# Kernel tuning notes

Measured on AMD Instinct MI355X. Metric: run time of the kernel, lower is better.

## Reference

```python
import jax, jax.numpy as jnp
import numpy as np

T, B, IN, H, L = 512, 32, 512, 512, 2  # seq_len, batch, input_size, hidden_size, num_layers
D = 2  # bidirectional
EPS = 1e-5


def setup_inputs() -> dict:
    key = jax.random.key(0)
    ks = jax.random.split(key, 4)
    s = 0.05
    return {
        "x": jax.random.normal(ks[0], (T, B, IN), jnp.float32),
        "h0": jnp.zeros((L * D, B, H), jnp.float32),
        # stacked per (layer, direction) params; index = 2*layer + dir (dir 0 = fwd, 1 = back)
        "Wx": jax.random.normal(ks[1], (L * D, IN, 3 * H), jnp.float32) * s,
        "Wh": jax.random.normal(ks[2], (L * D, H, 3 * H), jnp.float32) * s,
        "bx": jnp.zeros((L * D, 3 * H), jnp.float32),
        "bh": jnp.zeros((L * D, 3 * H), jnp.float32),
        "gx": jnp.ones((L * D, 3 * H), jnp.float32),   # LN affine scale for input proj
        "bex": jnp.zeros((L * D, 3 * H), jnp.float32), # LN affine shift for input proj
        "gh": jnp.ones((L * D, 3 * H), jnp.float32),   # LN affine scale for recurrent proj
        "beh": jnp.zeros((L * D, 3 * H), jnp.float32), # LN affine shift for recurrent proj
    }


def _ln3(a, g, b):
    # per-gate LayerNorm: a is [B, 3H]; normalize each H-sized gate chunk
    Bn, H3 = a.shape
    Hh = H3 // 3
    a = a.reshape(Bn, 3, Hh)
    mu = a.mean(-1, keepdims=True)
    var = ((a - mu) ** 2).mean(-1, keepdims=True)
    a = (a - mu) * jax.lax.rsqrt(var + EPS)
    a = a * g.reshape(3, Hh) + b.reshape(3, Hh)
    return a.reshape(Bn, H3)


def _run_dir(xs, h, Wx, Wh, bx, bh, gx, bex, gh, beh):
    # xs: [T, B, F], h: [B, H]; scan LNGRU cell over time
    def step(h, x):
        ax = _ln3(x @ Wx + bx, gx, bex)
        ah = _ln3(h @ Wh + bh, gh, beh)
        axr, axz, axn = jnp.split(ax, 3, axis=-1)
        ahr, ahz, ahn = jnp.split(ah, 3, axis=-1)
        r = jax.nn.sigmoid(axr + ahr)
        z = jax.nn.sigmoid(axz + ahz)
        n = jnp.tanh(axn + r * ahn)
        h_new = (1.0 - z) * n + z * h
        return h_new, h_new
    hT, ys = jax.lax.scan(step, h, xs)
    return hT, ys


def reference(x, h0, Wx, Wh, bx, bh, gx, bex, gh, beh):
    ff, back = x, x
    hiddens = []
    for layer in range(L):
        i = 2 * layer
        hT, ff = _run_dir(ff, h0[i], Wx[i], Wh[i], bx[i], bh[i], gx[i], bex[i], gh[i], beh[i])
        hiddens.append(hT)
        j = 2 * layer + 1
        hT, yb = _run_dir(back[::-1], h0[j], Wx[j], Wh[j], bx[j], bh[j], gx[j], bex[j], gh[j], beh[j])
        back = yb[::-1]
        hiddens.append(hT)
    output = jnp.concatenate([ff, back], axis=-1)  # [T, B, 2H]
    return output, jnp.stack(hiddens)  # hiddens: [L*2, B, H]
```

## Files before the change

kernel.cpp:

```cpp
#include <hip/hip_runtime.h>

#define T_N 512
#define B_N 32
#define H_N 512
#define G3 1536
#define NBLK 192
#define NGRP 8
#define GRPSZ (NBLK / NGRP)
#define NT 1024
#define EPS_LN 1e-5f
#define OUT_HID_OFF (T_N * B_N * 1024)

#define WS_STATS 320
#define WS_DOTS  (WS_STATS + 1536)
#define WS_HBUF  (WS_DOTS + 4 * B_N * G3)
#define WS_Y0    (WS_HBUF + 2 * B_N * H_N)

#define WLDS_F 32256
#define HL_F   8256
#define LDS_BYTES ((WLDS_F + HL_F + 256) * 4)

__device__ __forceinline__ float cload(const float* p) {
  return __hip_atomic_load(p, __ATOMIC_RELAXED, __HIP_MEMORY_SCOPE_AGENT);
}
__device__ __forceinline__ void cstore(float* p, float v) {
  __hip_atomic_store(p, v, __ATOMIC_RELAXED, __HIP_MEMORY_SCOPE_AGENT);
}
union U64F2 { unsigned long long u; float f[2]; };
__device__ __forceinline__ U64F2 cload2(const float* p) {
  U64F2 r;
  r.u = __hip_atomic_load((const unsigned long long*)p, __ATOMIC_RELAXED,
                          __HIP_MEMORY_SCOPE_AGENT);
  return r;
}

__device__ __forceinline__ void gbar(unsigned* barbase, unsigned& epoch, int grp) {
  epoch++;
  __builtin_amdgcn_s_waitcnt(0);
  __syncthreads();
  if (threadIdx.x == 0) {
    unsigned* gc  = barbase + grp * 32;
    unsigned* top = barbase + NGRP * 32;
    unsigned* rel = barbase + NGRP * 32 + 32;
    unsigned r = __hip_atomic_fetch_add(gc, 1u, __ATOMIC_RELAXED, __HIP_MEMORY_SCOPE_AGENT);
    if (r == epoch * GRPSZ - 1u) {
      unsigned r2 = __hip_atomic_fetch_add(top, 1u, __ATOMIC_RELAXED, __HIP_MEMORY_SCOPE_AGENT);
      if (r2 == epoch * NGRP - 1u)
        __hip_atomic_store(rel, epoch, __ATOMIC_RELAXED, __HIP_MEMORY_SCOPE_AGENT);
    }
    while (__hip_atomic_load(rel, __ATOMIC_RELAXED, __HIP_MEMORY_SCOPE_AGENT) < epoch)
      __builtin_amdgcn_s_sleep(1);
  }
  __syncthreads();
}

__global__ void __launch_bounds__(NT, 1)
lngru5(const float* __restrict__ x, const float* __restrict__ h0,
       const float* __restrict__ Wx, const float* __restrict__ Wh,
       const float* __restrict__ bx, const float* __restrict__ bh,
       const float* __restrict__ gx, const float* __restrict__ bex,
       const float* __restrict__ gh, const float* __restrict__ beh,
       float* __restrict__ out, float* __restrict__ ws)
{
  extern __shared__ __align__(16) float smem[];
  float* wlds = smem;
  float* hl   = smem + WLDS_F;
  float* sred = smem + WLDS_F + HL_F;

  unsigned* barbase = (unsigned*)ws;
  float* stats = ws + WS_STATS;
  float* dots  = ws + WS_DOTS;
  float* hbuf  = ws + WS_HBUF;
  float* y0    = ws + WS_Y0;

  const int tid  = threadIdx.x;
  const int lane = tid & 63;
  const int wv   = tid >> 6;
  const int bid  = blockIdx.x;
  const int grp  = bid & 7;
  const int bs   = bid & 1;
  const int jt   = (bid >> 1) % 24;
  const int kd   = (bid >> 1) / 24;
  const int kind = kd & 1;
  const int d    = kd >> 1;
  const int j0   = jt * 64;
  const int g    = jt >> 3;
  const int b0   = bs * 16;
  const bool is_gate = (kind == 0) && (jt < 8);

  const int jq    = wv >> 1;
  const int bhf   = wv & 1;
  const int jj    = lane & 7;
  const int boct  = lane >> 3;
  const int b_loc = bhf * 8 + boct;
  const int b     = b0 + b_loc;
  const int jfull = j0 + jq * 8 + jj;

  unsigned epoch = 0;

  for (int ph = 0; ph < 2; ++ph) {
    const int widx = ph * 2 + d;

    const float* wgl = (kind ? Wh : Wx) + (size_t)widx * H_N * G3 + j0;
    for (int kk = 0; kk < 32; ++kk) {
      int k = wv * 32 + kk;
      if (k < 504)
        wlds[(k >> 2) * 256 + lane * 4 + (k & 3)] = wgl[(size_t)k * G3 + lane];
    }
    float wtail[8];
#pragma unroll
    for (int kk = 0; kk < 8; ++kk)
      wtail[kk] = wgl[(size_t)(504 + kk) * G3 + (jq * 8 + jj)];

    if (is_gate) {
      cstore(&hbuf[(d * B_N + b0 + wv) * H_N + j0 + lane],
             h0[(widx * B_N + b0 + wv) * H_N + j0 + lane]);
    }
    gbar(barbase, epoch, grp);

    const float  bv   = (kind ? bh : bx)[widx * G3 + jfull];
    const float* xsrc = (ph == 0) ? x : (y0 + (size_t)d * T_N * B_N * H_N);
    const float* hsrc = hbuf + (d * B_N + b0) * H_N;
    const float4* wq  = (const float4*)wlds + jq * 8 + jj;

    for (int s = 0; s < T_N; ++s) {
      const int t = d ? (T_N - 1 - s) : s;
      const int p = s & 1;
      float* stp = stats + p * 768;

      if (kind) {
#pragma unroll
        for (int q = 0; q < 4; ++q) {
          int e = (tid + q * 1024) * 2;
          U64F2 v = cload2(hsrc + e);
          int bb = e >> 9, k = e & 511;
          hl[bb * 516 + k]     = v.f[0];
          hl[bb * 516 + k + 1] = v.f[1];
        }
        __syncthreads();
      }

      float p0 = 0.f, p1 = 0.f, p2 = 0.f, p3 = 0.f;
      if (kind) {
        const float* hb = hl + b_loc * 516;
#pragma unroll 9
        for (int k4 = 0; k4 < 126; ++k4) {
          float4 w = wq[k4 * 64];
          float4 r = *(const float4*)(hb + k4 * 4);
          p0 = fmaf(r.x, w.x, p0);
          p1 = fmaf(r.y, w.y, p1);
          p2 = fmaf(r.z, w.z, p2);
          p3 = fmaf(r.w, w.w, p3);
        }
        float4 r1 = *(const float4*)(hb + 504);
        float4 r2 = *(const float4*)(hb + 508);
        p0 = fmaf(r1.x, wtail[0], p0); p1 = fmaf(r1.y, wtail[1], p1);
        p2 = fmaf(r1.z, wtail[2], p2); p3 = fmaf(r1.w, wtail[3], p3);
        p0 = fmaf(r2.x, wtail[4], p0); p1 = fmaf(r2.y, wtail[5], p1);
        p2 = fmaf(r2.z, wtail[6], p2); p3 = fmaf(r2.w, wtail[7], p3);
      } else {
        const float* rp = xsrc + ((size_t)t * B_N + b) * H_N;
#pragma unroll 9
        for (int k4 = 0; k4 < 126; ++k4) {
          float4 w = wq[k4 * 64];
          float4 r = *(const float4*)(rp + k4 * 4);
          p0 = fmaf(r.x, w.x, p0);
          p1 = fmaf(r.y, w.y, p1);
          p2 = fmaf(r.z, w.z, p2);
          p3 = fmaf(r.w, w.w, p3);
        }
        float4 r1 = *(const float4*)(rp + 504);
        float4 r2 = *(const float4*)(rp + 508);
        p0 = fmaf(r1.x, wtail[0], p0); p1 = fmaf(r1.y, wtail[1], p1);
        p2 = fmaf(r1.z, wtail[2], p2); p3 = fmaf(r1.w, wtail[3], p3);
        p0 = fmaf(r2.x, wtail[4], p0); p1 = fmaf(r2.y, wtail[5], p1);
        p2 = fmaf(r2.z, wtail[6], p2); p3 = fmaf(r2.w, wtail[7], p3);
      }
      float tot = bv + (p0 + p1) + (p2 + p3);

      cstore(&dots[(kd * B_N + b) * G3 + jfull], tot);

      float s1 = tot, s2 = tot * tot;
      s1 += __shfl_xor(s1, 1, 64); s2 += __shfl_xor(s2, 1, 64);
      s1 += __shfl_xor(s1, 2, 64); s2 += __shfl_xor(s2, 2, 64);
      s1 += __shfl_xor(s1, 4, 64); s2 += __shfl_xor(s2, 4, 64);
      if (jj == 0) {
        sred[(wv * 8 + boct) * 2 + 0] = s1;
        sred[(wv * 8 + boct) * 2 + 1] = s2;
      }
      __syncthreads();
      if (tid < 32) {
        int bl = tid >> 1, st = tid & 1;
        int bh2 = bl >> 3, bo2 = bl & 7;
        float a2 = 0.f;
#pragma unroll
        for (int q = 0; q < 8; ++q) a2 += sred[((q * 2 + bh2) * 8 + bo2) * 2 + st];
        atomicAdd(&stp[((kd * 3 + g) * B_N + b0 + bl) * 2 + st], a2);
      }

      gbar(barbase, epoch, grp);

      if (bid == NBLK - 1) {
        float* so = stats + (p ^ 1) * 768;
        if (tid < 768) cstore(so + tid, 0.f);
      }
      if (is_gate) {
        const int c  = j0 + lane;
        const int gb = b0 + wv;
        float a[2][3];
#pragma unroll
        for (int k2 = 0; k2 < 2; ++k2) {
          const float* dr  = dots + ((d * 2 + k2) * B_N + gb) * G3;
          const float* gam = (k2 ? gh : gx) + widx * G3;
          const float* bet = (k2 ? beh : bex) + widx * G3;
#pragma unroll
          for (int g2 = 0; g2 < 3; ++g2) {
            float v = cload(dr + g2 * H_N + c);
            const float* sl = stp + (((d * 2 + k2) * 3 + g2) * B_N + gb) * 2;
            float mu  = cload(sl)     * (1.f / 512.f);
            float var = cload(sl + 1) * (1.f / 512.f) - mu * mu;
            float inv = rsqrtf(var + EPS_LN);
            int J = g2 * H_N + c;
            a[k2][g2] = (v - mu) * inv * gam[J] + bet[J];
          }
        }
        float r = 1.f / (1.f + __expf(-(a[0][0] + a[1][0])));
        float z = 1.f / (1.f + __expf(-(a[0][1] + a[1][1])));
        float n = tanhf(a[0][2] + r * a[1][2]);
        float* hp = hbuf + (d * B_N + gb) * H_N + c;
        float hnew = (1.f - z) * n + z * cload(hp);
        cstore(hp, hnew);
        if (ph == 0) {
          cstore(&y0[(((size_t)d * T_N + t) * B_N + gb) * H_N + c], hnew);
        } else {
          out[((size_t)t * B_N + gb) * 1024 + d * H_N + c] = hnew;
        }
        if (s == T_N - 1) {
          out[OUT_HID_OFF + (widx * B_N + gb) * H_N + c] = hnew;
        }
      }
      gbar(barbase, epoch, grp);
    }
  }
}

extern "C" void kernel_launch(void* const* d_in, const int* in_sizes, int n_in,
                              void* d_out, int out_size, void* d_ws, size_t ws_size,
                              hipStream_t stream) {
  const float* x    = (const float*)d_in[0];
  const float* h0   = (const float*)d_in[1];
  const float* Wx   = (const float*)d_in[2];
  const float* Wh   = (const float*)d_in[3];
  const float* bxp  = (const float*)d_in[4];
  const float* bhp  = (const float*)d_in[5];
  const float* gxp  = (const float*)d_in[6];
  const float* bexp = (const float*)d_in[7];
  const float* ghp  = (const float*)d_in[8];
  const float* behp = (const float*)d_in[9];
  float* out = (float*)d_out;
  float* ws  = (float*)d_ws;

  hipMemsetAsync(d_ws, 0, 8192, stream);

  hipFuncSetAttribute((const void*)lngru5,
                      hipFuncAttributeMaxDynamicSharedMemorySize, LDS_BYTES);

  void* args[] = {(void*)&x, (void*)&h0, (void*)&Wx, (void*)&Wh, (void*)&bxp, (void*)&bhp,
                  (void*)&gxp, (void*)&bexp, (void*)&ghp, (void*)&behp, (void*)&out, (void*)&ws};
  hipLaunchCooperativeKernel((void*)lngru5, dim3(NBLK), dim3(NT), args, LDS_BYTES, stream);
}
```

Baseline: 26.25 ms.

## Split K across waves with 4x4 register tiles and LDS atomic reduction

Restructures the per-step matvec so each wave handles a slice of the K dimension and computes a 4x4 (j, batch) register tile, reusing each loaded weight and activation float4 across four outputs. Partial sums are combined through LDS atomics into a per-block accumulator. The x rows are now staged into LDS like the hidden state instead of being read straight from global memory per thread. This cuts LDS and global load traffic per FMA, at the cost of LDS atomic contention, an extra barrier, and uneven K splits across waves.

```diff
diff --git a/kernel.cpp b/kernel.cpp
--- a/kernel.cpp
+++ b/kernel.cpp
@@ -16,9 +16,11 @@
 #define WS_HBUF  (WS_DOTS + 4 * B_N * G3)
 #define WS_Y0    (WS_HBUF + 2 * B_N * H_N)
 
-#define WLDS_F 32256
+#define WLDS_F 31232
 #define HL_F   8256
-#define LDS_BYTES ((WLDS_F + HL_F + 256) * 4)
+#define PACC_F 1024
+#define SRED_F 128
+#define LDS_BYTES ((WLDS_F + HL_F + PACC_F + SRED_F) * 4)
 
 __device__ __forceinline__ float cload(const float* p) {
   return __hip_atomic_load(p, __ATOMIC_RELAXED, __HIP_MEMORY_SCOPE_AGENT);
@@ -54,8 +56,12 @@
   __syncthreads();
 }
 
+#define DOT4(A, W, R) A = fmaf((W).x, (R).x, fmaf((W).y, (R).y, fmaf((W).z, (R).z, fmaf((W).w, (R).w, A))))
+#define ACC4(I, W) do { DOT4(acc[I][0], W, r0); DOT4(acc[I][1], W, r1); \
+                        DOT4(acc[I][2], W, r2); DOT4(acc[I][3], W, r3); } while (0)
+
 __global__ void __launch_bounds__(NT, 1)
-lngru5(const float* __restrict__ x, const float* __restrict__ h0,
+lngru7(const float* __restrict__ x, const float* __restrict__ h0,
        const float* __restrict__ Wx, const float* __restrict__ Wh,
        const float* __restrict__ bx, const float* __restrict__ bh,
        const float* __restrict__ gx, const float* __restrict__ bex,
@@ -65,7 +71,8 @@
   extern __shared__ __align__(16) float smem[];
   float* wlds = smem;
   float* hl   = smem + WLDS_F;
-  float* sred = smem + WLDS_F + HL_F;
+  float* pacc = smem + WLDS_F + HL_F;
+  float* sred = smem + WLDS_F + HL_F + PACC_F;
 
   unsigned* barbase = (unsigned*)ws;
   float* stats = ws + WS_STATS;
@@ -88,29 +95,38 @@
   const int b0   = bs * 16;
   const bool is_gate = (kind == 0) && (jt < 8);
 
-  const int jq    = wv >> 1;
-  const int bhf   = wv & 1;
-  const int jj    = lane & 7;
-  const int boct  = lane >> 3;
-  const int b_loc = bhf * 8 + boct;
-  const int b     = b0 + b_loc;
-  const int jfull = j0 + jq * 8 + jj;
+  const int jg = lane & 15;
+  const int bg = lane >> 4;
+  const int cnt = (wv < 10) ? 8 : 7;
+  const int k40 = (wv < 10) ? (wv * 8) : (80 + (wv - 10) * 7);
+  const int tk0 = 488 + (wv - 10) * 4;
+
+  const int jlo = (tid & 15) * 4 + (tid >> 8);
+  const int blo = ((tid >> 4) & 3) * 4 + ((tid >> 6) & 3);
 
   unsigned epoch = 0;
 
   for (int ph = 0; ph < 2; ++ph) {
     const int widx = ph * 2 + d;
 
+    pacc[tid] = 0.f;
+
     const float* wgl = (kind ? Wh : Wx) + (size_t)widx * H_N * G3 + j0;
-    for (int kk = 0; kk < 32; ++kk) {
-      int k = wv * 32 + kk;
-      if (k < 504)
-        wlds[(k >> 2) * 256 + lane * 4 + (k & 3)] = wgl[(size_t)k * G3 + lane];
-    }
-    float wtail[8];
-#pragma unroll
-    for (int kk = 0; kk < 8; ++kk)
-      wtail[kk] = wgl[(size_t)(504 + kk) * G3 + (jq * 8 + jj)];
+    for (int e = tid; e < 488 * 64; e += NT) {
+      int k = e >> 6, jl = e & 63;
+      wlds[(k >> 2) * 256 + (jl & 3) * 64 + (jl >> 2) * 4 + (k & 3)] =
+          wgl[(size_t)k * G3 + jl];
+    }
+    float4 wt[4];
+    if (wv >= 10) {
+#pragma unroll
+      for (int i = 0; i < 4; ++i) {
+        wt[i].x = wgl[(size_t)(tk0 + 0) * G3 + jg * 4 + i];
+        wt[i].y = wgl[(size_t)(tk0 + 1) * G3 + jg * 4 + i];
+        wt[i].z = wgl[(size_t)(tk0 + 2) * G3 + jg * 4 + i];
+        wt[i].w = wgl[(size_t)(tk0 + 3) * G3 + jg * 4 + i];
+      }
+    }
 
     if (is_gate) {
       cstore(&hbuf[(d * B_N + b0 + wv) * H_N + j0 + lane],
@@ -118,10 +134,11 @@
     }
     gbar(barbase, epoch, grp);
 
-    const float  bv   = (kind ? bh : bx)[widx * G3 + jfull];
+    const float  bv   = (kind ? bh : bx)[widx * G3 + j0 + jlo];
     const float* xsrc = (ph == 0) ? x : (y0 + (size_t)d * T_N * B_N * H_N);
     const float* hsrc = hbuf + (d * B_N + b0) * H_N;
-    const float4* wq  = (const float4*)wlds + jq * 8 + jj;
+    const float4* wp4 = (const float4*)wlds;
+    const float*  hb0 = hl + (bg * 4) * 516;
 
     for (int s = 0; s < T_N; ++s) {
       const int t = d ? (T_N - 1 - s) : s;
@@ -134,67 +151,72 @@
           int e = (tid + q * 1024) * 2;
           U64F2 v = cload2(hsrc + e);
           int bb = e >> 9, k = e & 511;
-          hl[bb * 516 + k]     = v.f[0];
-          hl[bb * 516 + k + 1] = v.f[1];
-        }
-        __syncthreads();
-      }
-
-      float p0 = 0.f, p1 = 0.f, p2 = 0.f, p3 = 0.f;
-      if (kind) {
-        const float* hb = hl + b_loc * 516;
-#pragma unroll 9
-        for (int k4 = 0; k4 < 126; ++k4) {
-          float4 w = wq[k4 * 64];
-          float4 r = *(const float4*)(hb + k4 * 4);
-          p0 = fmaf(r.x, w.x, p0);
-          p1 = fmaf(r.y, w.y, p1);
-          p2 = fmaf(r.z, w.z, p2);
-          p3 = fmaf(r.w, w.w, p3);
-        }
-        float4 r1 = *(const float4*)(hb + 504);
-        float4 r2 = *(const float4*)(hb + 508);
-        p0 = fmaf(r1.x, wtail[0], p0); p1 = fmaf(r1.y, wtail[1], p1);
-        p2 = fmaf(r1.z, wtail[2], p2); p3 = fmaf(r1.w, wtail[3], p3);
-        p0 = fmaf(r2.x, wtail[4], p0); p1 = fmaf(r2.y, wtail[5], p1);
-        p2 = fmaf(r2.z, wtail[6], p2); p3 = fmaf(r2.w, wtail[7], p3);
+          *(float2*)(hl + bb * 516 + k) = make_float2(v.f[0], v.f[1]);
+        }
       } else {
-        const float* rp = xsrc + ((size_t)t * B_N + b) * H_N;
-#pragma unroll 9
-        for (int k4 = 0; k4 < 126; ++k4) {
-          float4 w = wq[k4 * 64];
-          float4 r = *(const float4*)(rp + k4 * 4);
-          p0 = fmaf(r.x, w.x, p0);
-          p1 = fmaf(r.y, w.y, p1);
-          p2 = fmaf(r.z, w.z, p2);
-          p3 = fmaf(r.w, w.w, p3);
-        }
-        float4 r1 = *(const float4*)(rp + 504);
-        float4 r2 = *(const float4*)(rp + 508);
-        p0 = fmaf(r1.x, wtail[0], p0); p1 = fmaf(r1.y, wtail[1], p1);
-        p2 = fmaf(r1.z, wtail[2], p2); p3 = fmaf(r1.w, wtail[3], p3);
-        p0 = fmaf(r2.x, wtail[4], p0); p1 = fmaf(r2.y, wtail[5], p1);
-        p2 = fmaf(r2.z, wtail[6], p2); p3 = fmaf(r2.w, wtail[7], p3);
-      }
-      float tot = bv + (p0 + p1) + (p2 + p3);
-
-      cstore(&dots[(kd * B_N + b) * G3 + jfull], tot);
+        const float* xrow = xsrc + ((size_t)t * B_N + b0) * H_N;
+#pragma unroll
+        for (int q = 0; q < 2; ++q) {
+          int e = (tid + q * 1024) * 4;
+          float4 a = *(const float4*)(xrow + e);
+          int bb = e >> 9, k = e & 511;
+          *(float4*)(hl + bb * 516 + k) = a;
+        }
+      }
+      __syncthreads();
+
+      float acc[4][4] = {};
+#pragma unroll 2
+      for (int q = 0; q < cnt; ++q) {
+        const int k4 = k40 + q;
+        const float4* wp_ = wp4 + k4 * 64 + jg;
+        float4 w0 = wp_[0];
+        float4 w1 = wp_[16];
+        float4 w2 = wp_[32];
+        float4 w3 = wp_[48];
+        const float* hk_ = hb0 + k4 * 4;
+        float4 r0 = *(const float4*)(hk_);
+        float4 r1 = *(const float4*)(hk_ + 516);
+        float4 r2 = *(const float4*)(hk_ + 1032);
+        float4 r3 = *(const float4*)(hk_ + 1548);
+        ACC4(0, w0); ACC4(1, w1); ACC4(2, w2); ACC4(3, w3);
+      }
+      if (wv >= 10) {
+        const float* hk_ = hb0 + tk0;
+        float4 r0 = *(const float4*)(hk_);
+        float4 r1 = *(const float4*)(hk_ + 516);
+        float4 r2 = *(const float4*)(hk_ + 1032);
+        float4 r3 = *(const float4*)(hk_ + 1548);
+        ACC4(0, wt[0]); ACC4(1, wt[1]); ACC4(2, wt[2]); ACC4(3, wt[3]);
+      }
+
+#pragma unroll
+      for (int i = 0; i < 4; ++i)
+#pragma unroll
+        for (int m = 0; m < 4; ++m)
+          atomicAdd(&pacc[(i << 8) + (m << 6) + (bg << 4) + jg], acc[i][m]);
+      __syncthreads();
+
+      float tot = pacc[tid] + bv;
+      pacc[tid] = 0.f;
+      cstore(&dots[(kd * B_N + b0 + blo) * G3 + j0 + jlo], tot);
 
       float s1 = tot, s2 = tot * tot;
       s1 += __shfl_xor(s1, 1, 64); s2 += __shfl_xor(s2, 1, 64);
       s1 += __shfl_xor(s1, 2, 64); s2 += __shfl_xor(s2, 2, 64);
       s1 += __shfl_xor(s1, 4, 64); s2 += __shfl_xor(s2, 4, 64);
-      if (jj == 0) {
-        sred[(wv * 8 + boct) * 2 + 0] = s1;
-        sred[(wv * 8 + boct) * 2 + 1] = s2;
+      s1 += __shfl_xor(s1, 8, 64); s2 += __shfl_xor(s2, 8, 64);
+      if ((lane & 15) == 0) {
+        sred[(wv * 4 + (lane >> 4)) * 2 + 0] = s1;
+        sred[(wv * 4 + (lane >> 4)) * 2 + 1] = s2;
       }
       __syncthreads();
       if (tid < 32) {
         int bl = tid >> 1, st = tid & 1;
-        int bh2 = bl >> 3, bo2 = bl & 7;
+        int bgq = bl >> 2, mq = bl & 3;
         float a2 = 0.f;
 #pragma unroll
-        for (int q = 0; q < 8; ++q) a2 += sred[((q * 2 + bh2) * 8 + bo2) * 2 + st];
+        for (int i = 0; i < 4; ++i) a2 += sred[((i * 4 + mq) * 4 + bgq) * 2 + st];
         atomicAdd(&stp[((kd * 3 + g) * B_N + b0 + bl) * 2 + st], a2);
       }
 
@@ -262,10 +284,10 @@
 
   hipMemsetAsync(d_ws, 0, 8192, stream);
 
-  hipFuncSetAttribute((const void*)lngru5,
+  hipFuncSetAttribute((const void*)lngru7,
                       hipFuncAttributeMaxDynamicSharedMemorySize, LDS_BYTES);
 
   void* args[] = {(void*)&x, (void*)&h0, (void*)&Wx, (void*)&Wh, (void*)&bxp, (void*)&bhp,
                   (void*)&gxp, (void*)&bexp, (void*)&ghp, (void*)&behp, (void*)&out, (void*)&ws};
-  hipLaunchCooperativeKernel((void*)lngru5, dim3(NBLK), dim3(NT), args, LDS_BYTES, stream);
-}
+  hipLaunchCooperativeKernel((void*)lngru7, dim3(NBLK), dim3(NT), args, LDS_BYTES, stream);
+}
```

Result: slower. 36.63 ms (+39.5%).

## Register-block GEMV with 2x2 column/batch tile on half the waves

Applied to the files above, without the earlier changes.

Each thread now computes a 2x2 tile (two output columns by two batch rows) so every weight and input float4 loaded is reused twice. Only waves 0-3 do the matvec, while waves 4-15 sit idle until the reduction barrier. The aim is to cut LDS and global load traffic per FMA. The cost is lower wave-level parallelism and latency hiding, plus more register pressure from 16 accumulators.

```diff
diff --git a/kernel.cpp b/kernel.cpp
--- a/kernel.cpp
+++ b/kernel.cpp
@@ -54,8 +54,19 @@
   __syncthreads();
 }
 
+#define FMA16(WA, WB, R1, R2) do { \
+  acc[0][0][0]=fmaf((R1).x,(WA).x,acc[0][0][0]); acc[0][0][1]=fmaf((R1).y,(WA).y,acc[0][0][1]); \
+  acc[0][0][2]=fmaf((R1).z,(WA).z,acc[0][0][2]); acc[0][0][3]=fmaf((R1).w,(WA).w,acc[0][0][3]); \
+  acc[0][1][0]=fmaf((R2).x,(WA).x,acc[0][1][0]); acc[0][1][1]=fmaf((R2).y,(WA).y,acc[0][1][1]); \
+  acc[0][1][2]=fmaf((R2).z,(WA).z,acc[0][1][2]); acc[0][1][3]=fmaf((R2).w,(WA).w,acc[0][1][3]); \
+  acc[1][0][0]=fmaf((R1).x,(WB).x,acc[1][0][0]); acc[1][0][1]=fmaf((R1).y,(WB).y,acc[1][0][1]); \
+  acc[1][0][2]=fmaf((R1).z,(WB).z,acc[1][0][2]); acc[1][0][3]=fmaf((R1).w,(WB).w,acc[1][0][3]); \
+  acc[1][1][0]=fmaf((R2).x,(WB).x,acc[1][1][0]); acc[1][1][1]=fmaf((R2).y,(WB).y,acc[1][1][1]); \
+  acc[1][1][2]=fmaf((R2).z,(WB).z,acc[1][1][2]); acc[1][1][3]=fmaf((R2).w,(WB).w,acc[1][1][3]); \
+} while (0)
+
 __global__ void __launch_bounds__(NT, 1)
-lngru5(const float* __restrict__ x, const float* __restrict__ h0,
+lngru9(const float* __restrict__ x, const float* __restrict__ h0,
        const float* __restrict__ Wx, const float* __restrict__ Wh,
        const float* __restrict__ bx, const float* __restrict__ bh,
        const float* __restrict__ gx, const float* __restrict__ bex,
@@ -88,13 +99,12 @@
   const int b0   = bs * 16;
   const bool is_gate = (kind == 0) && (jt < 8);
 
-  const int jq    = wv >> 1;
-  const int bhf   = wv & 1;
-  const int jj    = lane & 7;
-  const int boct  = lane >> 3;
-  const int b_loc = bhf * 8 + boct;
-  const int b     = b0 + b_loc;
-  const int jfull = j0 + jq * 8 + jj;
+  const bool gw  = (wv < 4);
+  const int jq   = wv & 3;
+  const int jj   = lane & 7;
+  const int boct = lane >> 3;
+  const int jla  = jq * 8 + jj;
+  const int jlb  = jla + 32;
 
   unsigned epoch = 0;
 
@@ -107,10 +117,20 @@
       if (k < 504)
         wlds[(k >> 2) * 256 + lane * 4 + (k & 3)] = wgl[(size_t)k * G3 + lane];
     }
-    float wtail[8];
-#pragma unroll
-    for (int kk = 0; kk < 8; ++kk)
-      wtail[kk] = wgl[(size_t)(504 + kk) * G3 + (jq * 8 + jj)];
+    float4 wt[2][2];
+    if (gw) {
+#pragma unroll
+      for (int h = 0; h < 2; ++h) {
+        wt[0][h].x = wgl[(size_t)(504 + 4*h + 0) * G3 + jla];
+        wt[0][h].y = wgl[(size_t)(504 + 4*h + 1) * G3 + jla];
+        wt[0][h].z = wgl[(size_t)(504 + 4*h + 2) * G3 + jla];
+        wt[0][h].w = wgl[(size_t)(504 + 4*h + 3) * G3 + jla];
+        wt[1][h].x = wgl[(size_t)(504 + 4*h + 0) * G3 + jlb];
+        wt[1][h].y = wgl[(size_t)(504 + 4*h + 1) * G3 + jlb];
+        wt[1][h].z = wgl[(size_t)(504 + 4*h + 2) * G3 + jlb];
+        wt[1][h].w = wgl[(size_t)(504 + 4*h + 3) * G3 + jlb];
+      }
+    }
 
     if (is_gate) {
       cstore(&hbuf[(d * B_N + b0 + wv) * H_N + j0 + lane],
@@ -118,10 +138,14 @@
     }
     gbar(barbase, epoch, grp);
 
-    const float  bv   = (kind ? bh : bx)[widx * G3 + jfull];
+    const float  bva  = (kind ? bh : bx)[widx * G3 + j0 + jla];
+    const float  bvb  = (kind ? bh : bx)[widx * G3 + j0 + jlb];
     const float* xsrc = (ph == 0) ? x : (y0 + (size_t)d * T_N * B_N * H_N);
     const float* hsrc = hbuf + (d * B_N + b0) * H_N;
-    const float4* wq  = (const float4*)wlds + jq * 8 + jj;
+    const float4* wqa = (const float4*)wlds + jla;
+    const float4* wqb = (const float4*)wlds + jlb;
+    const float*  h1  = hl + boct * 516;
+    const float*  h2  = hl + (boct + 8) * 516;
 
     for (int s = 0; s < T_N; ++s) {
       const int t = d ? (T_N - 1 - s) : s;
@@ -140,61 +164,82 @@
         __syncthreads();
       }
 
-      float p0 = 0.f, p1 = 0.f, p2 = 0.f, p3 = 0.f;
-      if (kind) {
-        const float* hb = hl + b_loc * 516;
-#pragma unroll 9
-        for (int k4 = 0; k4 < 126; ++k4) {
-          float4 w = wq[k4 * 64];
-          float4 r = *(const float4*)(hb + k4 * 4);
-          p0 = fmaf(r.x, w.x, p0);
-          p1 = fmaf(r.y, w.y, p1);
-          p2 = fmaf(r.z, w.z, p2);
-          p3 = fmaf(r.w, w.w, p3);
-        }
-        float4 r1 = *(const float4*)(hb + 504);
-        float4 r2 = *(const float4*)(hb + 508);
-        p0 = fmaf(r1.x, wtail[0], p0); p1 = fmaf(r1.y, wtail[1], p1);
-        p2 = fmaf(r1.z, wtail[2], p2); p3 = fmaf(r1.w, wtail[3], p3);
-        p0 = fmaf(r2.x, wtail[4], p0); p1 = fmaf(r2.y, wtail[5], p1);
-        p2 = fmaf(r2.z, wtail[6], p2); p3 = fmaf(r2.w, wtail[7], p3);
-      } else {
-        const float* rp = xsrc + ((size_t)t * B_N + b) * H_N;
-#pragma unroll 9
-        for (int k4 = 0; k4 < 126; ++k4) {
-          float4 w = wq[k4 * 64];
-          float4 r = *(const float4*)(rp + k4 * 4);
-          p0 = fmaf(r.x, w.x, p0);
-          p1 = fmaf(r.y, w.y, p1);
-          p2 = fmaf(r.z, w.z, p2);
-          p3 = fmaf(r.w, w.w, p3);
-        }
-        float4 r1 = *(const float4*)(rp + 504);
-        float4 r2 = *(const float4*)(rp + 508);
-        p0 = fmaf(r1.x, wtail[0], p0); p1 = fmaf(r1.y, wtail[1], p1);
-        p2 = fmaf(r1.z, wtail[2], p2); p3 = fmaf(r1.w, wtail[3], p3);
-        p0 = fmaf(r2.x, wtail[4], p0); p1 = fmaf(r2.y, wtail[5], p1);
-        p2 = fmaf(r2.z, wtail[6], p2); p3 = fmaf(r2.w, wtail[7], p3);
-      }
-      float tot = bv + (p0 + p1) + (p2 + p3);
-
-      cstore(&dots[(kd * B_N + b) * G3 + jfull], tot);
-
-      float s1 = tot, s2 = tot * tot;
-      s1 += __shfl_xor(s1, 1, 64); s2 += __shfl_xor(s2, 1, 64);
-      s1 += __shfl_xor(s1, 2, 64); s2 += __shfl_xor(s2, 2, 64);
-      s1 += __shfl_xor(s1, 4, 64); s2 += __shfl_xor(s2, 4, 64);
-      if (jj == 0) {
-        sred[(wv * 8 + boct) * 2 + 0] = s1;
-        sred[(wv * 8 + boct) * 2 + 1] = s2;
+      float acc[2][2][4] = {{{0.f,0.f,0.f,0.f},{0.f,0.f,0.f,0.f}},
+                            {{0.f,0.f,0.f,0.f},{0.f,0.f,0.f,0.f}}};
+      if (gw) {
+        if (kind) {
+#pragma unroll 3
+          for (int k4 = 0; k4 < 126; ++k4) {
+            float4 wa = wqa[k4 * 64];
+            float4 wb = wqb[k4 * 64];
+            float4 r1 = *(const float4*)(h1 + k4 * 4);
+            float4 r2 = *(const float4*)(h2 + k4 * 4);
+            FMA16(wa, wb, r1, r2);
+          }
+          {
+            float4 r1a = *(const float4*)(h1 + 504);
+            float4 r1b = *(const float4*)(h1 + 508);
+            float4 r2a = *(const float4*)(h2 + 504);
+            float4 r2b = *(const float4*)(h2 + 508);
+            FMA16(wt[0][0], wt[1][0], r1a, r2a);
+            FMA16(wt[0][1], wt[1][1], r1b, r2b);
+          }
+        } else {
+          const float* rp1 = xsrc + ((size_t)t * B_N + b0 + boct) * H_N;
+          const float* rp2 = rp1 + 8 * H_N;
+#pragma unroll 6
+          for (int k4 = 0; k4 < 126; ++k4) {
+            float4 wa = wqa[k4 * 64];
+            float4 wb = wqb[k4 * 64];
+            float4 r1 = *(const float4*)(rp1 + k4 * 4);
+            float4 r2 = *(const float4*)(rp2 + k4 * 4);
+            FMA16(wa, wb, r1, r2);
+          }
+          {
+            float4 r1a = *(const float4*)(rp1 + 504);
+            float4 r1b = *(const float4*)(rp1 + 508);
+            float4 r2a = *(const float4*)(rp2 + 504);
+            float4 r2b = *(const float4*)(rp2 + 508);
+            FMA16(wt[0][0], wt[1][0], r1a, r2a);
+            FMA16(wt[0][1], wt[1][1], r1b, r2b);
+          }
+        }
+      }
+
+      if (gw) {
+        float ta1 = bva + (acc[0][0][0] + acc[0][0][1]) + (acc[0][0][2] + acc[0][0][3]);
+        float ta2 = bva + (acc[0][1][0] + acc[0][1][1]) + (acc[0][1][2] + acc[0][1][3]);
+        float tb1 = bvb + (acc[1][0][0] + acc[1][0][1]) + (acc[1][0][2] + acc[1][0][3]);
+        float tb2 = bvb + (acc[1][1][0] + acc[1][1][1]) + (acc[1][1][2] + acc[1][1][3]);
+
+        float* dr1 = &dots[(size_t)(kd * B_N + b0 + boct) * G3 + j0];
+        float* dr2 = dr1 + (size_t)8 * G3;
+        cstore(dr1 + jla, ta1);
+        cstore(dr1 + jlb, tb1);
+        cstore(dr2 + jla, ta2);
+        cstore(dr2 + jlb, tb2);
+
+        float s1a = ta1 + tb1, s2a = ta1 * ta1 + tb1 * tb1;
+        float s1b = ta2 + tb2, s2b = ta2 * ta2 + tb2 * tb2;
+        s1a += __shfl_xor(s1a, 1, 64); s2a += __shfl_xor(s2a, 1, 64);
+        s1b += __shfl_xor(s1b, 1, 64); s2b += __shfl_xor(s2b, 1, 64);
+        s1a += __shfl_xor(s1a, 2, 64); s2a += __shfl_xor(s2a, 2, 64);
+        s1b += __shfl_xor(s1b, 2, 64); s2b += __shfl_xor(s2b, 2, 64);
+        s1a += __shfl_xor(s1a, 4, 64); s2a += __shfl_xor(s2a, 4, 64);
+        s1b += __shfl_xor(s1b, 4, 64); s2b += __shfl_xor(s2b, 4, 64);
+        if (jj == 0) {
+          sred[(boct * 4 + jq) * 2 + 0] = s1a;
+          sred[(boct * 4 + jq) * 2 + 1] = s2a;
+          sred[((boct + 8) * 4 + jq) * 2 + 0] = s1b;
+          sred[((boct + 8) * 4 + jq) * 2 + 1] = s2b;
+        }
       }
       __syncthreads();
       if (tid < 32) {
         int bl = tid >> 1, st = tid & 1;
-        int bh2 = bl >> 3, bo2 = bl & 7;
         float a2 = 0.f;
 #pragma unroll
-        for (int q = 0; q < 8; ++q) a2 += sred[((q * 2 + bh2) * 8 + bo2) * 2 + st];
+        for (int q = 0; q < 4; ++q) a2 += sred[(bl * 4 + q) * 2 + st];
         atomicAdd(&stp[((kd * 3 + g) * B_N + b0 + bl) * 2 + st], a2);
       }
 
@@ -262,10 +307,10 @@
 
   hipMemsetAsync(d_ws, 0, 8192, stream);
 
-  hipFuncSetAttribute((const void*)lngru5,
+  hipFuncSetAttribute((const void*)lngru9,
                       hipFuncAttributeMaxDynamicSharedMemorySize, LDS_BYTES);
 
   void* args[] = {(void*)&x, (void*)&h0, (void*)&Wx, (void*)&Wh, (void*)&bxp, (void*)&bhp,
                   (void*)&gxp, (void*)&bexp, (void*)&ghp, (void*)&behp, (void*)&out, (void*)&ws};
-  hipLaunchCooperativeKernel((void*)lngru5, dim3(NBLK), dim3(NT), args, LDS_BYTES, stream);
-}
+  hipLaunchCooperativeKernel((void*)lngru9, dim3(NBLK), dim3(NT), args, LDS_BYTES, stream);
+}
```

Result: faster. 22.21 ms (-15.4%).
